# Kernel optimization log

Measured on AMD Instinct MI355X. Metric: run time of the kernel, lower is better.

The kernel has to match this reference:

```python
import jax, jax.numpy as jnp
import numpy as np

N = 50000
E = 800000
IN_DIM = 64          # 'in_dim'; ndata h has dim 2*in_dim, p has dim in_dim
EDGE_DIM = 32
OUT_DIM = 64
AVG_D_LOG = 2.8332   # avg_d['log'] = log(avg_degree + 1), avg_degree = 16
EPS_STD = 1e-5
EPS_BN = 1e-5


def setup_inputs() -> dict:
    key = jax.random.key(0)
    ks = jax.random.split(key, 16)
    def glorot(k, fan_in, fan_out):
        lim = np.sqrt(6.0 / (fan_in + fan_out)).astype(np.float32)
        return jax.random.uniform(k, (fan_in, fan_out), jnp.float32, -lim, lim)
    d_pre_h = 2 * 2 * IN_DIM + EDGE_DIM   # 288
    d_pre_p = 2 * IN_DIM + EDGE_DIM       # 160
    d_post_h = (4 * 3 + 2) * IN_DIM       # 896
    d_post_p = (4 * 3 + 1) * IN_DIM       # 832
    return {
        "h": jax.random.normal(ks[0], (N, 2 * IN_DIM), jnp.float32),
        "p": jax.random.normal(ks[1], (N, IN_DIM), jnp.float32),
        "e": jax.random.normal(ks[2], (E, EDGE_DIM), jnp.float32),
        "src": jax.random.randint(ks[3], (E,), 0, N, jnp.int32),
        "dst": jax.random.randint(ks[4], (E,), 0, N, jnp.int32),
        "snorm_n": jax.random.uniform(ks[5], (N, 1), jnp.float32, 0.05, 1.0),
        "W_pre_h": glorot(ks[6], d_pre_h, IN_DIM),
        "b_pre_h": jnp.zeros((IN_DIM,), jnp.float32),
        "W_pre_p": glorot(ks[7], d_pre_p, IN_DIM),
        "b_pre_p": jnp.zeros((IN_DIM,), jnp.float32),
        "W_post_h": glorot(ks[8], d_post_h, OUT_DIM),
        "b_post_h": jnp.zeros((OUT_DIM,), jnp.float32),
        "W_post_p": glorot(ks[9], d_post_p, OUT_DIM),
        "b_post_p": jnp.zeros((OUT_DIM,), jnp.float32),
        "bn_gamma": jnp.ones((OUT_DIM,), jnp.float32),
        "bn_beta": jnp.zeros((OUT_DIM,), jnp.float32),
    }


def _agg_scale(msg, dst, deg):
    # msg: [E, d] edge messages reduced at dst; PNA aggregators mean/max/min/std
    degc = jnp.maximum(deg, 1.0)
    s = jax.ops.segment_sum(msg, dst, num_segments=N)
    mean = s / degc[:, None]
    sq = jax.ops.segment_sum(msg * msg, dst, num_segments=N) / degc[:, None]
    var = jax.nn.relu(sq - mean * mean)
    std = jnp.sqrt(var + EPS_STD)
    has = (deg > 0)[:, None]
    mx = jnp.where(has, jax.ops.segment_max(msg, dst, num_segments=N), 0.0)
    mn = jnp.where(has, jax.ops.segment_min(msg, dst, num_segments=N), 0.0)
    agg = jnp.concatenate([mean, mx, mn, std], axis=1)  # [N, 4d]
    logd = jnp.where(deg > 0, jnp.log(deg + 1.0), 1.0)
    amp = (logd / AVG_D_LOG)[:, None]
    att = (AVG_D_LOG / logd)[:, None]
    # scalers: identity, amplification, attenuation -> [N, 12d]
    return jnp.concatenate([agg, agg * amp, agg * att], axis=1)


def reference(h, p, e, src, dst, snorm_n,
              W_pre_h, b_pre_h, W_pre_p, b_pre_p,
              W_post_h, b_post_h, W_post_p, b_post_p,
              bn_gamma, bn_beta):
    # pretrans (1-layer MLP == linear) on concatenated edge endpoint features
    z_h = jnp.concatenate([h[src], h[dst], e], axis=1)   # [E, 4*in+edge]
    z_p = jnp.concatenate([p[src], p[dst], e], axis=1)   # [E, 2*in+edge]
    e_for_h = z_h @ W_pre_h + b_pre_h                    # [E, in]
    e_for_p = z_p @ W_pre_p + b_pre_p                    # [E, in]

    deg = jax.ops.segment_sum(jnp.ones((E,), jnp.float32), dst, num_segments=N)
    agg_h = _agg_scale(e_for_h, dst, deg)                # [N, 12*in]
    agg_p = _agg_scale(e_for_p, dst, deg)                # [N, 12*in]

    h_cat = jnp.concatenate([h, agg_h], axis=1)          # [N, 14*in]
    p_cat = jnp.concatenate([p, agg_p], axis=1)          # [N, 13*in]
    h_out = h_cat @ W_post_h + b_post_h                  # [N, out]
    p_out = p_cat @ W_post_p + b_post_p                  # [N, out]

    # graph norm
    h_out = h_out * snorm_n
    # batch norm (training-mode batch statistics, biased variance)
    mu = jnp.mean(h_out, axis=0)
    var = jnp.mean((h_out - mu) ** 2, axis=0)
    h_out = (h_out - mu) / jnp.sqrt(var + EPS_BN) * bn_gamma + bn_beta
    # dropout = identity (eval / p=0)
    return h_out, p_out
```

## Files before the change

### kernel.cpp

```cpp
#include <hip/hip_runtime.h>
#include <hip/hip_bf16.h>
#include <hip/hip_fp16.h>


#define N_NODES 50000
#define N_EDGES 800000
#define NS 3200000
#define AVG_D_LOG 2.8332f

typedef unsigned short u16;
typedef unsigned int u32;
typedef __attribute__((ext_vector_type(8))) short short8;
typedef __attribute__((ext_vector_type(4))) float f32x4;

__device__ __forceinline__ float bflo(u32 u) { return __uint_as_float(u << 16); }
__device__ __forceinline__ float bfhi(u32 u) { return __uint_as_float(u & 0xffff0000u); }
__device__ __forceinline__ float bf2f(u16 u) { return __uint_as_float(((u32)u) << 16); }
__device__ __forceinline__ u16 f2bf(float x) {
  u32 u = __float_as_uint(x);
  return (u16)((u + 0x7fff + ((u >> 16) & 1)) >> 16);
}
__device__ __forceinline__ u16 f2h(float x) { return __half_as_ushort(__float2half(x)); }
__device__ __forceinline__ float h2f(u16 x) { return __half2float(__ushort_as_half(x)); }

__device__ __forceinline__ int is_bf(const void* gamma) {
  return ((const u32*)gamma)[0] == 0x3F803F80u ? 1 : 0;
}

__device__ __forceinline__ f32x4 mfma16(short8 a, short8 b, f32x4 c) {
  return __builtin_amdgcn_mfma_f32_16x16x32_bf16(a, b, c, 0, 0, 0);
}

__device__ __forceinline__ void load8(float z[8], const void* base, size_t off,
                                      int bf) {
  if (bf) {
    uint4 u = *(const uint4*)((const u16*)base + off);
    z[0] = bflo(u.x); z[1] = bfhi(u.x); z[2] = bflo(u.y); z[3] = bfhi(u.y);
    z[4] = bflo(u.z); z[5] = bfhi(u.z); z[6] = bflo(u.w); z[7] = bfhi(u.w);
  } else {
    const float* f = (const float*)base + off;
    float4 a = *(const float4*)f;
    float4 b = *(const float4*)(f + 4);
    z[0] = a.x; z[1] = a.y; z[2] = a.z; z[3] = a.w;
    z[4] = b.x; z[5] = b.y; z[6] = b.z; z[7] = b.w;
  }
}

__device__ __forceinline__ float load1(const void* base, size_t off, int bf) {
  return bf ? bf2f(((const u16*)base)[off]) : ((const float*)base)[off];
}

__global__ __launch_bounds__(256) void k_init(int* __restrict__ cnt,
                                              float* __restrict__ bnacc) {
  int i = blockIdx.x * 256 + threadIdx.x;
  if (i < N_NODES) cnt[i] = 0;
  else if (i < N_NODES + 128) bnacc[i - N_NODES] = 0.0f;
}

__global__ __launch_bounds__(256) void k_convert(
    const void* __restrict__ Wpreh, const void* __restrict__ Wprep,
    const void* __restrict__ Wposth, const void* __restrict__ Wpostp,
    const void* __restrict__ bpreh, const void* __restrict__ bprep,
    const void* __restrict__ bposth, const void* __restrict__ bpostp,
    const void* __restrict__ gamma, float* __restrict__ bias,
    u16* __restrict__ frag) {
  int i = blockIdx.x * 256 + threadIdx.x;
  if (i >= 256 + 139264) return;
  int bf = is_bf(gamma);
  if (i < 256) {
    const void* s = (i < 64) ? bpreh : (i < 128) ? bprep : (i < 192) ? bposth : bpostp;
    bias[i] = load1(s, i & 63, bf);
    return;
  }
  int g = i - 256;
  const void* W; int fidx, rowoff;
  if (g < 8192)        { W = Wpreh;  fidx = g;          rowoff = 0; }
  else if (g < 16384)  { W = Wpreh;  fidx = g - 8192;   rowoff = 128; }
  else if (g < 20480)  { W = Wprep;  fidx = g - 16384;  rowoff = 0; }
  else if (g < 24576)  { W = Wprep;  fidx = g - 20480;  rowoff = 64; }
  else if (g < 81920)  { W = Wposth; fidx = g - 24576;  rowoff = 0; }
  else if (g < 135168) { W = Wpostp; fidx = g - 81920;  rowoff = 0; }
  else if (g < 137216) { W = Wpreh;  fidx = g - 135168; rowoff = 256; }
  else                 { W = Wprep;  fidx = g - 137216; rowoff = 128; }
  int f = fidx;
  int kc = f >> 11, nt = (f >> 9) & 3, lane = (f >> 3) & 63, j = f & 7;
  int k = kc * 32 + (lane >> 4) * 8 + j;
  int n = nt * 16 + (lane & 15);
  frag[g] = f2bf(load1(W, (size_t)(rowoff + k) * 64 + n, bf));
}

__global__ __launch_bounds__(256) void k_hist(const int* __restrict__ dst,
                                              int* __restrict__ cnt) {
  int i = blockIdx.x * 256 + threadIdx.x;
  if (i < N_EDGES) atomicAdd(cnt + dst[i], 1);
}

__global__ __launch_bounds__(1024) void k_scan1(const int* __restrict__ cnt,
                                                int* __restrict__ offs,
                                                int* __restrict__ bsum) {
  __shared__ int buf[1024];
  int t = threadIdx.x;
  int i = blockIdx.x * 1024 + t;
  int v = (i < N_NODES) ? cnt[i] : 0;
  buf[t] = v;
  __syncthreads();
#pragma unroll
  for (int d = 1; d < 1024; d <<= 1) {
    int x = (t >= d) ? buf[t - d] : 0;
    __syncthreads();
    buf[t] += x;
    __syncthreads();
  }
  if (i < N_NODES) offs[i] = buf[t] - v;
  if (t == 1023) bsum[blockIdx.x] = buf[1023];
}
__global__ void k_scan2(const int* __restrict__ bsum, int* __restrict__ boff,
                        int* __restrict__ offs, int nb) {
  if (threadIdx.x == 0 && blockIdx.x == 0) {
    int run = 0;
    for (int b = 0; b < nb; ++b) { boff[b] = run; run += bsum[b]; }
    offs[N_NODES] = run;
  }
}
__global__ __launch_bounds__(256) void k_scan3(int* __restrict__ offs,
                                               const int* __restrict__ boff,
                                               int* __restrict__ cnt) {
  int i = blockIdx.x * 256 + threadIdx.x;
  if (i < N_NODES) {
    int v = offs[i] + boff[i >> 10];
    offs[i] = v;
    cnt[i] = v;
  }
}

__global__ __launch_bounds__(256) void k_order(const int* __restrict__ src,
                                               const int* __restrict__ dst,
                                               int* __restrict__ cnt,
                                               int* __restrict__ peid,
                                               int* __restrict__ psrc) {
  int i = blockIdx.x * 256 + threadIdx.x;
  if (i < N_EDGES) {
    int pos = atomicAdd(cnt + dst[i], 1);
    peid[pos] = i;
    psrc[pos] = src[i];
  }
}

__global__ __launch_bounds__(256) void k_uproj(
    const void* __restrict__ h, const void* __restrict__ p,
    const float* __restrict__ bias, const u16* __restrict__ frag,
    const void* __restrict__ gamma, u16* __restrict__ Uhs,
    u16* __restrict__ Uhd, u16* __restrict__ Ups, u16* __restrict__ Upd) {
  int wid = (blockIdx.x * 256 + threadIdx.x) >> 6;
  int lane = threadIdx.x & 63;
  if (wid >= 12500) return;
  int part = wid / 3125;
  int node0 = (wid % 3125) * 16;
  int bf = is_bf(gamma);
  const void* feat = (part < 2) ? h : p;
  int pitch = (part < 2) ? 128 : 64;
  int kcn = (part < 2) ? 4 : 2;
  const u16* bfr = frag + (part == 0 ? 0 : part == 1 ? 8192 : part == 2 ? 16384 : 20480);
  u16* U = part == 0 ? Uhs : part == 1 ? Uhd : part == 2 ? Ups : Upd;
  int m = lane & 15, quad = lane >> 4;
  f32x4 acc[4];
#pragma unroll
  for (int nt = 0; nt < 4; ++nt) acc[nt] = (f32x4){0.f, 0.f, 0.f, 0.f};
#pragma unroll
  for (int kc = 0; kc < 4; ++kc) {
    if (kc >= kcn) break;
    float z[8];
    load8(z, feat, (size_t)(node0 + m) * pitch + kc * 32 + quad * 8, bf);
    short8 a;
#pragma unroll
    for (int q = 0; q < 8; ++q) a[q] = (short)f2bf(z[q]);
#pragma unroll
    for (int nt = 0; nt < 4; ++nt) {
      short8 b = *(const short8*)(bfr + (size_t)((kc * 4 + nt) * 64 + lane) * 8);
      acc[nt] = mfma16(a, b, acc[nt]);
    }
  }
  const float* bv = (part == 1) ? bias : (part == 3) ? bias + 64 : nullptr;
#pragma unroll
  for (int r = 0; r < 4; ++r) {
    int node = node0 + quad * 4 + r;
#pragma unroll
    for (int nt = 0; nt < 4; ++nt) {
      int col = nt * 16 + m;
      float v = acc[nt][r] + (bv ? bv[col] : 0.f);
      U[(size_t)node * 64 + col] = f2h(v);
    }
  }
}

template <int BF>
__global__ __launch_bounds__(256) void k_emsg(
    const void* __restrict__ e, const u16* __restrict__ Wf,
    const int* __restrict__ peid, const void* __restrict__ gamma,
    u16* __restrict__ M) {
  if (is_bf(gamma) != BF) return;
  int wid = (blockIdx.x * 256 + threadIdx.x) >> 6;
  int lane = threadIdx.x & 63;
  if (wid >= N_EDGES / 16) return;
  int m = lane & 15, quad = lane >> 4;
  int pos0 = wid * 16;
  int eid = peid[pos0 + m];
  float z[8];
  load8(z, e, (size_t)eid * 32 + quad * 8, BF);
  short8 a;
#pragma unroll
  for (int q = 0; q < 8; ++q) a[q] = (short)f2bf(z[q]);
  f32x4 acc[4];
#pragma unroll
  for (int nt = 0; nt < 4; ++nt) acc[nt] = (f32x4){0.f, 0.f, 0.f, 0.f};
#pragma unroll
  for (int nt = 0; nt < 4; ++nt) {
    short8 b = *(const short8*)(Wf + (size_t)(nt * 64 + lane) * 8);
    acc[nt] = mfma16(a, b, acc[nt]);
  }
#pragma unroll
  for (int r = 0; r < 4; ++r) {
    size_t pos = pos0 + quad * 4 + r;
#pragma unroll
    for (int nt = 0; nt < 4; ++nt)
      M[pos * 64 + nt * 16 + m] = f2h(acc[nt][r]);
  }
}

template <int BF, int FC>
__global__ __launch_bounds__(256, 4) void k_agg(
    const void* __restrict__ feat, const int* __restrict__ psrc,
    const int* __restrict__ offs, const u16* __restrict__ Us,
    const u16* __restrict__ Ud, const u16* __restrict__ M,
    const void* __restrict__ gamma, u16* __restrict__ A,
    float* __restrict__ degf) {
  if (is_bf(gamma) != BF) return;
  int n = blockIdx.x * 4 + (threadIdx.x >> 6);
  int lane = threadIdx.x & 63;
  if (n >= N_NODES) return;
  int s = offs[n], epos = offs[n + 1];
  float udv = h2f(Ud[(size_t)n * 64 + lane]);
  float sum = 0.f, sq = 0.f, mx = -3.4e38f, mn = 3.4e38f;
  int i = s;
  for (; i + 3 < epos; i += 4) {
    int s0 = __builtin_amdgcn_readfirstlane(psrc[i]);
    int s1 = __builtin_amdgcn_readfirstlane(psrc[i + 1]);
    int s2 = __builtin_amdgcn_readfirstlane(psrc[i + 2]);
    int s3 = __builtin_amdgcn_readfirstlane(psrc[i + 3]);
    float m0 = udv + h2f(Us[(size_t)s0 * 64 + lane]) + h2f(M[(size_t)i * 64 + lane]);
    float m1 = udv + h2f(Us[(size_t)s1 * 64 + lane]) + h2f(M[(size_t)(i + 1) * 64 + lane]);
    float m2 = udv + h2f(Us[(size_t)s2 * 64 + lane]) + h2f(M[(size_t)(i + 2) * 64 + lane]);
    float m3 = udv + h2f(Us[(size_t)s3 * 64 + lane]) + h2f(M[(size_t)(i + 3) * 64 + lane]);
    sum += (m0 + m1) + (m2 + m3);
    sq = fmaf(m0, m0, fmaf(m1, m1, fmaf(m2, m2, fmaf(m3, m3, sq))));
    mx = fmaxf(fmaxf(mx, m0), fmaxf(fmaxf(m1, m2), m3));
    mn = fminf(fminf(mn, m0), fminf(fminf(m1, m2), m3));
  }
  for (; i < epos; ++i) {
    int s0 = __builtin_amdgcn_readfirstlane(psrc[i]);
    float m0 = udv + h2f(Us[(size_t)s0 * 64 + lane]) + h2f(M[(size_t)i * 64 + lane]);
    sum += m0; sq = fmaf(m0, m0, sq);
    mx = fmaxf(mx, m0); mn = fminf(mn, m0);
  }
  float dv = (float)(epos - s);
  bool has = dv > 0.5f;
  float inv = has ? 1.f / dv : 1.f;
  if (lane == 0) degf[n] = dv;
  float mean = sum * inv;
  float var = fmaf(-mean, mean, sq * inv);
  var = var > 0.f ? var : 0.f;
  float vals[4] = {mean, has ? mx : 0.f, has ? mn : 0.f, sqrtf(var + 1e-5f)};
  u16* Arow = A + (size_t)n * (FC * 64 + 256);
#pragma unroll
  for (int c = 0; c < FC; ++c)
    Arow[c * 64 + lane] = f2bf(load1(feat, (size_t)n * (FC * 64) + c * 64 + lane, BF));
#pragma unroll
  for (int v2 = 0; v2 < 4; ++v2)
    Arow[FC * 64 + v2 * 64 + lane] = f2bf(vals[v2]);
}

__global__ __launch_bounds__(256) void k_node(
    const u16* __restrict__ Ah, const u16* __restrict__ Ap,
    const void* __restrict__ snorm, const float* __restrict__ degf,
    const u16* __restrict__ BfH, const u16* __restrict__ BfP,
    const float* __restrict__ biasH, const float* __restrict__ biasP,
    const void* __restrict__ gamma, float* __restrict__ outh,
    float* __restrict__ outp) {
  int w = (blockIdx.x * 256 + threadIdx.x) >> 6;
  int lane = threadIdx.x & 63;
  if (w >= N_NODES / 16) return;
  int bf = is_bf(gamma);
  int m = lane & 15, quad = lane >> 4;
  int node0 = w * 16;

  float ampr[4], attr[4];
#pragma unroll
  for (int r = 0; r < 4; ++r) {
    float dv = degf[node0 + quad * 4 + r];
    float logd = (dv > 0.5f) ? logf(dv + 1.f) : 1.f;
    ampr[r] = logd * (1.f / AVG_D_LOG);
    attr[r] = AVG_D_LOG / logd;
  }

  f32x4 accB[4], accA[4], accT[4];
#pragma unroll
  for (int nt = 0; nt < 4; ++nt) {
    accB[nt] = (f32x4){0.f, 0.f, 0.f, 0.f};
    accA[nt] = (f32x4){0.f, 0.f, 0.f, 0.f};
    accT[nt] = (f32x4){0.f, 0.f, 0.f, 0.f};
  }
#pragma unroll 2
  for (int kc = 0; kc < 12; ++kc) {
    short8 a = *(const short8*)(Ah + (size_t)(node0 + m) * 384 + kc * 32 + quad * 8);
#pragma unroll
    for (int nt = 0; nt < 4; ++nt)
      accB[nt] = mfma16(a, *(const short8*)(BfH + (size_t)((kc * 4 + nt) * 64 + lane) * 8), accB[nt]);
    if (kc >= 4) {
      int kk = kc - 4;
#pragma unroll
      for (int nt = 0; nt < 4; ++nt)
        accA[nt] = mfma16(a, *(const short8*)(BfH + 24576 + (size_t)((kk * 4 + nt) * 64 + lane) * 8), accA[nt]);
#pragma unroll
      for (int nt = 0; nt < 4; ++nt)
        accT[nt] = mfma16(a, *(const short8*)(BfH + 40960 + (size_t)((kk * 4 + nt) * 64 + lane) * 8), accT[nt]);
    }
  }
  float bH[4];
#pragma unroll
  for (int nt = 0; nt < 4; ++nt) bH[nt] = biasH[nt * 16 + m];
#pragma unroll
  for (int r = 0; r < 4; ++r) {
    int node = node0 + quad * 4 + r;
    float sn = load1(snorm, node, bf);
#pragma unroll
    for (int nt = 0; nt < 4; ++nt) {
      float v = accB[nt][r] + ampr[r] * accA[nt][r] + attr[r] * accT[nt][r] + bH[nt];
      outh[(size_t)node * 64 + nt * 16 + m] = v * sn;
    }
  }

#pragma unroll
  for (int nt = 0; nt < 4; ++nt) {
    accB[nt] = (f32x4){0.f, 0.f, 0.f, 0.f};
    accA[nt] = (f32x4){0.f, 0.f, 0.f, 0.f};
    accT[nt] = (f32x4){0.f, 0.f, 0.f, 0.f};
  }
#pragma unroll 2
  for (int kc = 0; kc < 10; ++kc) {
    short8 a = *(const short8*)(Ap + (size_t)(node0 + m) * 320 + kc * 32 + quad * 8);
#pragma unroll
    for (int nt = 0; nt < 4; ++nt)
      accB[nt] = mfma16(a, *(const short8*)(BfP + (size_t)((kc * 4 + nt) * 64 + lane) * 8), accB[nt]);
    if (kc >= 2) {
      int kk = kc - 2;
#pragma unroll
      for (int nt = 0; nt < 4; ++nt)
        accA[nt] = mfma16(a, *(const short8*)(BfP + 20480 + (size_t)((kk * 4 + nt) * 64 + lane) * 8), accA[nt]);
#pragma unroll
      for (int nt = 0; nt < 4; ++nt)
        accT[nt] = mfma16(a, *(const short8*)(BfP + 36864 + (size_t)((kk * 4 + nt) * 64 + lane) * 8), accT[nt]);
    }
  }
  float bP[4];
#pragma unroll
  for (int nt = 0; nt < 4; ++nt) bP[nt] = biasP[nt * 16 + m];
#pragma unroll
  for (int r = 0; r < 4; ++r) {
    int node = node0 + quad * 4 + r;
#pragma unroll
    for (int nt = 0; nt < 4; ++nt) {
      float v = accB[nt][r] + ampr[r] * accA[nt][r] + attr[r] * accT[nt][r] + bP[nt];
      outp[(size_t)node * 64 + nt * 16 + m] = v;
    }
  }
}

__global__ __launch_bounds__(256) void k_bnstats(const float* __restrict__ hpre,
                                                 float* __restrict__ bnacc) {
  int j = threadIdx.x & 63;
  float s = 0.0f, q = 0.0f;
  for (int n = blockIdx.x * 4 + (threadIdx.x >> 6); n < N_NODES;
       n += gridDim.x * 4) {
    float x = hpre[(size_t)n * 64 + j];
    s += x; q += x * x;
  }
  __shared__ float ls[256], lq[256];
  ls[threadIdx.x] = s; lq[threadIdx.x] = q;
  __syncthreads();
  if (threadIdx.x < 64) {
    s = ls[threadIdx.x] + ls[threadIdx.x + 64] + ls[threadIdx.x + 128] + ls[threadIdx.x + 192];
    q = lq[threadIdx.x] + lq[threadIdx.x + 64] + lq[threadIdx.x + 128] + lq[threadIdx.x + 192];
    atomicAdd(bnacc + threadIdx.x, s);
    atomicAdd(bnacc + 64 + threadIdx.x, q);
  }
}

__global__ __launch_bounds__(256) void k_bnapply(
    float* __restrict__ outh, const float* __restrict__ bnacc,
    const void* __restrict__ gamma, const void* __restrict__ beta) {
  int i = blockIdx.x * 256 + threadIdx.x;
  if (i >= NS) return;
  int bf = is_bf(gamma);
  int j = i & 63;
  const float invN = 1.0f / (float)N_NODES;
  float mu = bnacc[j] * invN;
  float var = fmaf(-mu, mu, bnacc[64 + j] * invN);
  var = var > 0.0f ? var : 0.0f;
  float sc = load1(gamma, j, bf) * rsqrtf(var + 1e-5f);
  float sh = load1(beta, j, bf) - mu * sc;
  outh[i] = fmaf(outh[i], sc, sh);
}

extern "C" void kernel_launch(void* const* d_in, const int* in_sizes, int n_in,
                              void* d_out, int out_size, void* d_ws,
                              size_t ws_size, hipStream_t stream) {
  const void* h = d_in[0];
  const void* p = d_in[1];
  const void* e = d_in[2];
  const int* src = (const int*)d_in[3];
  const int* dst = (const int*)d_in[4];
  const void* snorm = d_in[5];
  const void* Wpreh = d_in[6];
  const void* bpreh = d_in[7];
  const void* Wprep = d_in[8];
  const void* bprep = d_in[9];
  const void* Wposth = d_in[10];
  const void* bposth = d_in[11];
  const void* Wpostp = d_in[12];
  const void* bpostp = d_in[13];
  const void* gamma = d_in[14];
  const void* beta = d_in[15];

  float* ws = (float*)d_ws;
  u16* Uhs = (u16*)ws;
  u16* Uhd = Uhs + 3200000;
  u16* Ups = Uhd + 3200000;
  u16* Upd = Ups + 3200000;
  u16* M = (u16*)(ws + 6400000L);
  u16* Ah = (u16*)(ws + 32000000L);
  u16* Ap = (u16*)(ws + 41600000L);
  int* peid = (int*)(ws + 49600000L);
  int* psrc = (int*)(ws + 50400000L);
  int* cnt = (int*)(ws + 51200000L);
  int* offs = (int*)(ws + 51250000L);
  float* degf = ws + 51300004L;
  int* bsum = (int*)(ws + 51350004L);
  int* boff = (int*)(ws + 51350068L);
  float* bnacc = ws + 51350132L;
  float* bias = ws + 51350260L;
  u16* frag = (u16*)(ws + 51350516L);

  u16* fragPostH = frag + 24576;
  u16* fragPostP = frag + 81920;
  u16* fragWehF = frag + 135168;
  u16* fragWepF = frag + 137216;

  float* outh = (float*)d_out;
  float* outp = outh + (size_t)NS;

  k_init<<<(N_NODES + 128 + 255) / 256, 256, 0, stream>>>(cnt, bnacc);
  k_convert<<<(256 + 139264 + 255) / 256, 256, 0, stream>>>(
      Wpreh, Wprep, Wposth, Wpostp, bpreh, bprep, bposth, bpostp, gamma, bias,
      frag);
  k_hist<<<(N_EDGES + 255) / 256, 256, 0, stream>>>(dst, cnt);
  const int NB = (N_NODES + 1023) / 1024;
  k_scan1<<<NB, 1024, 0, stream>>>(cnt, offs, bsum);
  k_scan2<<<1, 64, 0, stream>>>(bsum, boff, offs, NB);
  k_scan3<<<(N_NODES + 255) / 256, 256, 0, stream>>>(offs, boff, cnt);
  k_order<<<(N_EDGES + 255) / 256, 256, 0, stream>>>(src, dst, cnt, peid, psrc);
  k_uproj<<<(12500 + 3) / 4, 256, 0, stream>>>(h, p, bias, frag, gamma, Uhs,
                                               Uhd, Ups, Upd);
  k_emsg<0><<<(N_EDGES / 16 + 3) / 4, 256, 0, stream>>>(e, fragWehF, peid,
                                                        gamma, M);
  k_emsg<1><<<(N_EDGES / 16 + 3) / 4, 256, 0, stream>>>(e, fragWehF, peid,
                                                        gamma, M);
  k_agg<0, 2><<<(N_NODES + 3) / 4, 256, 0, stream>>>(h, psrc, offs, Uhs, Uhd,
                                                     M, gamma, Ah, degf);
  k_agg<1, 2><<<(N_NODES + 3) / 4, 256, 0, stream>>>(h, psrc, offs, Uhs, Uhd,
                                                     M, gamma, Ah, degf);
  k_emsg<0><<<(N_EDGES / 16 + 3) / 4, 256, 0, stream>>>(e, fragWepF, peid,
                                                        gamma, M);
  k_emsg<1><<<(N_EDGES / 16 + 3) / 4, 256, 0, stream>>>(e, fragWepF, peid,
                                                        gamma, M);
  k_agg<0, 1><<<(N_NODES + 3) / 4, 256, 0, stream>>>(p, psrc, offs, Ups, Upd,
                                                     M, gamma, Ap, degf);
  k_agg<1, 1><<<(N_NODES + 3) / 4, 256, 0, stream>>>(p, psrc, offs, Ups, Upd,
                                                     M, gamma, Ap, degf);
  k_node<<<(N_NODES / 16 + 3) / 4, 256, 0, stream>>>(
      Ah, Ap, snorm, degf, fragPostH, fragPostP, bias + 128, bias + 192, gamma,
      outh, outp);
  k_bnstats<<<256, 256, 0, stream>>>(outh, bnacc);
  k_bnapply<<<(NS + 255) / 256, 256, 0, stream>>>(outh, bnacc, gamma, beta);
}
```

Baseline: 625.5 us.

## Fuse edge-message GEMM into aggregation and read node features directly in post-GEMM

Edge messages e@W_e are now computed inside the aggregation kernel with MFMA per 16-edge chunk, for both h and p in one pass, instead of being written to and reread from an E×64 half-precision buffer in separate kernels. Edge id and source are packed into one int2 array. The h/p copies into the A matrices are dropped, and k_node loads raw features directly. Host-side dtype detection via input sizes skips launching the unused bf16/fp32 variant. This cuts global traffic and launches, but raises register pressure (occupancy hint lowered to 3) and wastes work on padded chunks for low-degree nodes.

```diff
diff --git a/kernel.cpp b/kernel.cpp
--- a/kernel.cpp
+++ b/kernel.cpp
@@ -136,13 +136,11 @@
 __global__ __launch_bounds__(256) void k_order(const int* __restrict__ src,
                                                const int* __restrict__ dst,
                                                int* __restrict__ cnt,
-                                               int* __restrict__ peid,
-                                               int* __restrict__ psrc) {
+                                               int2* __restrict__ epack) {
   int i = blockIdx.x * 256 + threadIdx.x;
   if (i < N_EDGES) {
     int pos = atomicAdd(cnt + dst[i], 1);
-    peid[pos] = i;
-    psrc[pos] = src[i];
+    epack[pos] = make_int2(i, src[i]);
   }
 }
 
@@ -194,92 +192,164 @@
 }
 
 template <int BF>
-__global__ __launch_bounds__(256) void k_emsg(
-    const void* __restrict__ e, const u16* __restrict__ Wf,
-    const int* __restrict__ peid, const void* __restrict__ gamma,
-    u16* __restrict__ M) {
-  if (is_bf(gamma) != BF) return;
-  int wid = (blockIdx.x * 256 + threadIdx.x) >> 6;
-  int lane = threadIdx.x & 63;
-  if (wid >= N_EDGES / 16) return;
-  int m = lane & 15, quad = lane >> 4;
-  int pos0 = wid * 16;
-  int eid = peid[pos0 + m];
-  float z[8];
-  load8(z, e, (size_t)eid * 32 + quad * 8, BF);
-  short8 a;
-#pragma unroll
-  for (int q = 0; q < 8; ++q) a[q] = (short)f2bf(z[q]);
-  f32x4 acc[4];
-#pragma unroll
-  for (int nt = 0; nt < 4; ++nt) acc[nt] = (f32x4){0.f, 0.f, 0.f, 0.f};
-#pragma unroll
-  for (int nt = 0; nt < 4; ++nt) {
-    short8 b = *(const short8*)(Wf + (size_t)(nt * 64 + lane) * 8);
-    acc[nt] = mfma16(a, b, acc[nt]);
-  }
-#pragma unroll
-  for (int r = 0; r < 4; ++r) {
-    size_t pos = pos0 + quad * 4 + r;
-#pragma unroll
-    for (int nt = 0; nt < 4; ++nt)
-      M[pos * 64 + nt * 16 + m] = f2h(acc[nt][r]);
-  }
-}
-
-template <int BF, int FC>
-__global__ __launch_bounds__(256, 4) void k_agg(
-    const void* __restrict__ feat, const int* __restrict__ psrc,
-    const int* __restrict__ offs, const u16* __restrict__ Us,
-    const u16* __restrict__ Ud, const u16* __restrict__ M,
-    const void* __restrict__ gamma, u16* __restrict__ A,
-    float* __restrict__ degf) {
+__global__ __launch_bounds__(256, 3) void k_aggf(
+    const void* __restrict__ e, const int2* __restrict__ epack,
+    const int* __restrict__ offs, const u16* __restrict__ Uhs,
+    const u16* __restrict__ Uhd, const u16* __restrict__ Ups,
+    const u16* __restrict__ Upd, const u16* __restrict__ Wfh,
+    const u16* __restrict__ Wfp, const void* __restrict__ gamma,
+    u16* __restrict__ Ah, u16* __restrict__ Ap, float* __restrict__ degf) {
   if (is_bf(gamma) != BF) return;
   int n = blockIdx.x * 4 + (threadIdx.x >> 6);
   int lane = threadIdx.x & 63;
   if (n >= N_NODES) return;
+  int m = lane & 15, quad = lane >> 4;
   int s = offs[n], epos = offs[n + 1];
-  float udv = h2f(Ud[(size_t)n * 64 + lane]);
-  float sum = 0.f, sq = 0.f, mx = -3.4e38f, mn = 3.4e38f;
-  int i = s;
-  for (; i + 3 < epos; i += 4) {
-    int s0 = __builtin_amdgcn_readfirstlane(psrc[i]);
-    int s1 = __builtin_amdgcn_readfirstlane(psrc[i + 1]);
-    int s2 = __builtin_amdgcn_readfirstlane(psrc[i + 2]);
-    int s3 = __builtin_amdgcn_readfirstlane(psrc[i + 3]);
-    float m0 = udv + h2f(Us[(size_t)s0 * 64 + lane]) + h2f(M[(size_t)i * 64 + lane]);
-    float m1 = udv + h2f(Us[(size_t)s1 * 64 + lane]) + h2f(M[(size_t)(i + 1) * 64 + lane]);
-    float m2 = udv + h2f(Us[(size_t)s2 * 64 + lane]) + h2f(M[(size_t)(i + 2) * 64 + lane]);
-    float m3 = udv + h2f(Us[(size_t)s3 * 64 + lane]) + h2f(M[(size_t)(i + 3) * 64 + lane]);
-    sum += (m0 + m1) + (m2 + m3);
-    sq = fmaf(m0, m0, fmaf(m1, m1, fmaf(m2, m2, fmaf(m3, m3, sq))));
-    mx = fmaxf(fmaxf(mx, m0), fmaxf(fmaxf(m1, m2), m3));
-    mn = fminf(fminf(mn, m0), fminf(fminf(m1, m2), m3));
-  }
-  for (; i < epos; ++i) {
-    int s0 = __builtin_amdgcn_readfirstlane(psrc[i]);
-    float m0 = udv + h2f(Us[(size_t)s0 * 64 + lane]) + h2f(M[(size_t)i * 64 + lane]);
-    sum += m0; sq = fmaf(m0, m0, sq);
-    mx = fmaxf(mx, m0); mn = fminf(mn, m0);
-  }
-  float dv = (float)(epos - s);
-  bool has = dv > 0.5f;
+  int deg = epos - s;
+
+  short8 bh[4], bp[4];
+#pragma unroll
+  for (int nt = 0; nt < 4; ++nt) {
+    bh[nt] = *(const short8*)(Wfh + (size_t)(nt * 64 + lane) * 8);
+    bp[nt] = *(const short8*)(Wfp + (size_t)(nt * 64 + lane) * 8);
+  }
+  float uhd[4], upd[4];
+#pragma unroll
+  for (int nt = 0; nt < 4; ++nt) {
+    uhd[nt] = h2f(Uhd[(size_t)n * 64 + nt * 16 + m]);
+    upd[nt] = h2f(Upd[(size_t)n * 64 + nt * 16 + m]);
+  }
+  float hsum[4], hsq[4], hmx[4], hmn[4], psum[4], psq[4], pmx[4], pmn[4];
+#pragma unroll
+  for (int nt = 0; nt < 4; ++nt) {
+    hsum[nt] = hsq[nt] = psum[nt] = psq[nt] = 0.f;
+    hmx[nt] = pmx[nt] = -3.4e38f;
+    hmn[nt] = pmn[nt] = 3.4e38f;
+  }
+
+  for (int c0 = 0; c0 < deg; c0 += 16) {
+    int im = s + c0 + m; im = im < epos ? im : epos - 1;
+    int eid = epack[im].x;
+    int sce0, sce1, sce2, sce3;
+    {
+      int b0 = s + c0 + quad * 4;
+      int i0 = b0 < epos ? b0 : epos - 1;
+      int i1 = b0 + 1 < epos ? b0 + 1 : epos - 1;
+      int i2 = b0 + 2 < epos ? b0 + 2 : epos - 1;
+      int i3 = b0 + 3 < epos ? b0 + 3 : epos - 1;
+      sce0 = epack[i0].y; sce1 = epack[i1].y;
+      sce2 = epack[i2].y; sce3 = epack[i3].y;
+    }
+    float z[8];
+    load8(z, e, (size_t)eid * 32 + quad * 8, BF);
+    short8 a;
+#pragma unroll
+    for (int q = 0; q < 8; ++q) a[q] = (short)f2bf(z[q]);
+
+    {
+      f32x4 acc[4];
+#pragma unroll
+      for (int nt = 0; nt < 4; ++nt)
+        acc[nt] = mfma16(a, bh[nt], (f32x4){0.f, 0.f, 0.f, 0.f});
+      float us[4][4];
+#pragma unroll
+      for (int nt = 0; nt < 4; ++nt) {
+        us[0][nt] = h2f(Uhs[(size_t)sce0 * 64 + nt * 16 + m]);
+        us[1][nt] = h2f(Uhs[(size_t)sce1 * 64 + nt * 16 + m]);
+        us[2][nt] = h2f(Uhs[(size_t)sce2 * 64 + nt * 16 + m]);
+        us[3][nt] = h2f(Uhs[(size_t)sce3 * 64 + nt * 16 + m]);
+      }
+#pragma unroll
+      for (int r = 0; r < 4; ++r) {
+        bool valid = (c0 + quad * 4 + r) < deg;
+#pragma unroll
+        for (int nt = 0; nt < 4; ++nt) {
+          float v = acc[nt][r] + uhd[nt] + us[r][nt];
+          float vv = valid ? v : 0.f;
+          hsum[nt] += vv;
+          hsq[nt] = fmaf(vv, vv, hsq[nt]);
+          hmx[nt] = valid ? fmaxf(hmx[nt], v) : hmx[nt];
+          hmn[nt] = valid ? fminf(hmn[nt], v) : hmn[nt];
+        }
+      }
+    }
+    {
+      f32x4 acc[4];
+#pragma unroll
+      for (int nt = 0; nt < 4; ++nt)
+        acc[nt] = mfma16(a, bp[nt], (f32x4){0.f, 0.f, 0.f, 0.f});
+      float us[4][4];
+#pragma unroll
+      for (int nt = 0; nt < 4; ++nt) {
+        us[0][nt] = h2f(Ups[(size_t)sce0 * 64 + nt * 16 + m]);
+        us[1][nt] = h2f(Ups[(size_t)sce1 * 64 + nt * 16 + m]);
+        us[2][nt] = h2f(Ups[(size_t)sce2 * 64 + nt * 16 + m]);
+        us[3][nt] = h2f(Ups[(size_t)sce3 * 64 + nt * 16 + m]);
+      }
+#pragma unroll
+      for (int r = 0; r < 4; ++r) {
+        bool valid = (c0 + quad * 4 + r) < deg;
+#pragma unroll
+        for (int nt = 0; nt < 4; ++nt) {
+          float v = acc[nt][r] + upd[nt] + us[r][nt];
+          float vv = valid ? v : 0.f;
+          psum[nt] += vv;
+          psq[nt] = fmaf(vv, vv, psq[nt]);
+          pmx[nt] = valid ? fmaxf(pmx[nt], v) : pmx[nt];
+          pmn[nt] = valid ? fminf(pmn[nt], v) : pmn[nt];
+        }
+      }
+    }
+  }
+
+  float dv = (float)deg;
+  bool has = deg > 0;
   float inv = has ? 1.f / dv : 1.f;
   if (lane == 0) degf[n] = dv;
-  float mean = sum * inv;
-  float var = fmaf(-mean, mean, sq * inv);
-  var = var > 0.f ? var : 0.f;
-  float vals[4] = {mean, has ? mx : 0.f, has ? mn : 0.f, sqrtf(var + 1e-5f)};
-  u16* Arow = A + (size_t)n * (FC * 64 + 256);
-#pragma unroll
-  for (int c = 0; c < FC; ++c)
-    Arow[c * 64 + lane] = f2bf(load1(feat, (size_t)n * (FC * 64) + c * 64 + lane, BF));
-#pragma unroll
-  for (int v2 = 0; v2 < 4; ++v2)
-    Arow[FC * 64 + v2 * 64 + lane] = f2bf(vals[v2]);
+
+#pragma unroll
+  for (int nt = 0; nt < 4; ++nt) {
+    hsum[nt] += __shfl_xor(hsum[nt], 16); hsum[nt] += __shfl_xor(hsum[nt], 32);
+    hsq[nt] += __shfl_xor(hsq[nt], 16);   hsq[nt] += __shfl_xor(hsq[nt], 32);
+    hmx[nt] = fmaxf(hmx[nt], __shfl_xor(hmx[nt], 16));
+    hmx[nt] = fmaxf(hmx[nt], __shfl_xor(hmx[nt], 32));
+    hmn[nt] = fminf(hmn[nt], __shfl_xor(hmn[nt], 16));
+    hmn[nt] = fminf(hmn[nt], __shfl_xor(hmn[nt], 32));
+    psum[nt] += __shfl_xor(psum[nt], 16); psum[nt] += __shfl_xor(psum[nt], 32);
+    psq[nt] += __shfl_xor(psq[nt], 16);   psq[nt] += __shfl_xor(psq[nt], 32);
+    pmx[nt] = fmaxf(pmx[nt], __shfl_xor(pmx[nt], 16));
+    pmx[nt] = fmaxf(pmx[nt], __shfl_xor(pmx[nt], 32));
+    pmn[nt] = fminf(pmn[nt], __shfl_xor(pmn[nt], 16));
+    pmn[nt] = fminf(pmn[nt], __shfl_xor(pmn[nt], 32));
+  }
+
+#pragma unroll
+  for (int nt = 0; nt < 4; ++nt) {
+    {
+      float mean = hsum[nt] * inv;
+      float var = fmaf(-mean, mean, hsq[nt] * inv);
+      var = var > 0.f ? var : 0.f;
+      float sd = sqrtf(var + 1e-5f);
+      float v1 = has ? hmx[nt] : 0.f;
+      float v2 = has ? hmn[nt] : 0.f;
+      float o = quad == 0 ? mean : quad == 1 ? v1 : quad == 2 ? v2 : sd;
+      Ah[(size_t)n * 256 + quad * 64 + nt * 16 + m] = f2bf(o);
+    }
+    {
+      float mean = psum[nt] * inv;
+      float var = fmaf(-mean, mean, psq[nt] * inv);
+      var = var > 0.f ? var : 0.f;
+      float sd = sqrtf(var + 1e-5f);
+      float v1 = has ? pmx[nt] : 0.f;
+      float v2 = has ? pmn[nt] : 0.f;
+      float o = quad == 0 ? mean : quad == 1 ? v1 : quad == 2 ? v2 : sd;
+      Ap[(size_t)n * 256 + quad * 64 + nt * 16 + m] = f2bf(o);
+    }
+  }
 }
 
 __global__ __launch_bounds__(256) void k_node(
+    const void* __restrict__ h, const void* __restrict__ p,
     const u16* __restrict__ Ah, const u16* __restrict__ Ap,
     const void* __restrict__ snorm, const float* __restrict__ degf,
     const u16* __restrict__ BfH, const u16* __restrict__ BfP,
@@ -311,7 +381,15 @@
   }
 #pragma unroll 2
   for (int kc = 0; kc < 12; ++kc) {
-    short8 a = *(const short8*)(Ah + (size_t)(node0 + m) * 384 + kc * 32 + quad * 8);
+    short8 a;
+    if (kc < 4) {
+      float z[8];
+      load8(z, h, (size_t)(node0 + m) * 128 + kc * 32 + quad * 8, bf);
+#pragma unroll
+      for (int q = 0; q < 8; ++q) a[q] = (short)f2bf(z[q]);
+    } else {
+      a = *(const short8*)(Ah + (size_t)(node0 + m) * 256 + (kc - 4) * 32 + quad * 8);
+    }
 #pragma unroll
     for (int nt = 0; nt < 4; ++nt)
       accB[nt] = mfma16(a, *(const short8*)(BfH + (size_t)((kc * 4 + nt) * 64 + lane) * 8), accB[nt]);
@@ -347,7 +425,15 @@
   }
 #pragma unroll 2
   for (int kc = 0; kc < 10; ++kc) {
-    short8 a = *(const short8*)(Ap + (size_t)(node0 + m) * 320 + kc * 32 + quad * 8);
+    short8 a;
+    if (kc < 2) {
+      float z[8];
+      load8(z, p, (size_t)(node0 + m) * 64 + kc * 32 + quad * 8, bf);
+#pragma unroll
+      for (int q = 0; q < 8; ++q) a[q] = (short)f2bf(z[q]);
+    } else {
+      a = *(const short8*)(Ap + (size_t)(node0 + m) * 256 + (kc - 2) * 32 + quad * 8);
+    }
 #pragma unroll
     for (int nt = 0; nt < 4; ++nt)
       accB[nt] = mfma16(a, *(const short8*)(BfP + (size_t)((kc * 4 + nt) * 64 + lane) * 8), accB[nt]);
@@ -436,19 +522,17 @@
   u16* Uhd = Uhs + 3200000;
   u16* Ups = Uhd + 3200000;
   u16* Upd = Ups + 3200000;
-  u16* M = (u16*)(ws + 6400000L);
-  u16* Ah = (u16*)(ws + 32000000L);
-  u16* Ap = (u16*)(ws + 41600000L);
-  int* peid = (int*)(ws + 49600000L);
-  int* psrc = (int*)(ws + 50400000L);
-  int* cnt = (int*)(ws + 51200000L);
-  int* offs = (int*)(ws + 51250000L);
-  float* degf = ws + 51300004L;
-  int* bsum = (int*)(ws + 51350004L);
-  int* boff = (int*)(ws + 51350068L);
-  float* bnacc = ws + 51350132L;
-  float* bias = ws + 51350260L;
-  u16* frag = (u16*)(ws + 51350516L);
+  u16* Ah = (u16*)(ws + 6400000L);
+  u16* Ap = (u16*)(ws + 12800000L);
+  int2* epack = (int2*)(ws + 19200000L);
+  int* cnt = (int*)(ws + 20800016L);
+  int* offs = (int*)(ws + 20850016L);
+  float* degf = ws + 20900020L;
+  int* bsum = (int*)(ws + 20950020L);
+  int* boff = (int*)(ws + 20950084L);
+  float* bnacc = ws + 20950148L;
+  float* bias = ws + 20950276L;
+  u16* frag = (u16*)(ws + 20950532L);
 
   u16* fragPostH = frag + 24576;
   u16* fragPostP = frag + 81920;
@@ -457,6 +541,12 @@
 
   float* outh = (float*)d_out;
   float* outp = outh + (size_t)NS;
+
+  int bfh = -1;
+  if (in_sizes && n_in >= 16) {
+    if (in_sizes[0] == 25600000) bfh = 0;
+    else if (in_sizes[0] == 12800000) bfh = 1;
+  }
 
   k_init<<<(N_NODES + 128 + 255) / 256, 256, 0, stream>>>(cnt, bnacc);
   k_convert<<<(256 + 139264 + 255) / 256, 256, 0, stream>>>(
@@ -467,28 +557,20 @@
   k_scan1<<<NB, 1024, 0, stream>>>(cnt, offs, bsum);
   k_scan2<<<1, 64, 0, stream>>>(bsum, boff, offs, NB);
   k_scan3<<<(N_NODES + 255) / 256, 256, 0, stream>>>(offs, boff, cnt);
-  k_order<<<(N_EDGES + 255) / 256, 256, 0, stream>>>(src, dst, cnt, peid, psrc);
+  k_order<<<(N_EDGES + 255) / 256, 256, 0, stream>>>(src, dst, cnt, epack);
   k_uproj<<<(12500 + 3) / 4, 256, 0, stream>>>(h, p, bias, frag, gamma, Uhs,
                                                Uhd, Ups, Upd);
-  k_emsg<0><<<(N_EDGES / 16 + 3) / 4, 256, 0, stream>>>(e, fragWehF, peid,
-                                                        gamma, M);
-  k_emsg<1><<<(N_EDGES / 16 + 3) / 4, 256, 0, stream>>>(e, fragWehF, peid,
-                                                        gamma, M);
-  k_agg<0, 2><<<(N_NODES + 3) / 4, 256, 0, stream>>>(h, psrc, offs, Uhs, Uhd,
-                                                     M, gamma, Ah, degf);
-  k_agg<1, 2><<<(N_NODES + 3) / 4, 256, 0, stream>>>(h, psrc, offs, Uhs, Uhd,
-                                                     M, gamma, Ah, degf);
-  k_emsg<0><<<(N_EDGES / 16 + 3) / 4, 256, 0, stream>>>(e, fragWepF, peid,
-                                                        gamma, M);
-  k_emsg<1><<<(N_EDGES / 16 + 3) / 4, 256, 0, stream>>>(e, fragWepF, peid,
-                                                        gamma, M);
-  k_agg<0, 1><<<(N_NODES + 3) / 4, 256, 0, stream>>>(p, psrc, offs, Ups, Upd,
-                                                     M, gamma, Ap, degf);
-  k_agg<1, 1><<<(N_NODES + 3) / 4, 256, 0, stream>>>(p, psrc, offs, Ups, Upd,
-                                                     M, gamma, Ap, degf);
+  if (bfh != 1)
+    k_aggf<0><<<(N_NODES + 3) / 4, 256, 0, stream>>>(
+        e, epack, offs, Uhs, Uhd, Ups, Upd, fragWehF, fragWepF, gamma, Ah, Ap,
+        degf);
+  if (bfh != 0)
+    k_aggf<1><<<(N_NODES + 3) / 4, 256, 0, stream>>>(
+        e, epack, offs, Uhs, Uhd, Ups, Upd, fragWehF, fragWepF, gamma, Ah, Ap,
+        degf);
   k_node<<<(N_NODES / 16 + 3) / 4, 256, 0, stream>>>(
-      Ah, Ap, snorm, degf, fragPostH, fragPostP, bias + 128, bias + 192, gamma,
-      outh, outp);
+      h, p, Ah, Ap, snorm, degf, fragPostH, fragPostP, bias + 128, bias + 192,
+      gamma, outh, outp);
   k_bnstats<<<256, 256, 0, stream>>>(outh, bnacc);
   k_bnapply<<<(NS + 255) / 256, 256, 0, stream>>>(outh, bnacc, gamma, beta);
 }
```

New measurement: 517.1 us. -17.3%, faster.
